# Performance work log

Measured on AMD Instinct MI355X. Metric: run time of the kernel, lower is better.

Reference implementation:

```python
import jax, jax.numpy as jnp
import numpy as np

B, S, D = 4, 2048, 256
H = 8
HD = D // H
DFF = 512
EPS_CUTOFF = 1e-15
LN_EPS = 1e-5


def _layer_norm(x, gamma, beta):
    mu = jnp.mean(x, axis=-1, keepdims=True)
    var = jnp.mean(jnp.square(x - mu), axis=-1, keepdims=True)
    return (x - mu) * jax.lax.rsqrt(var + LN_EPS) * gamma + beta


def setup_inputs() -> dict:
    key = jax.random.key(0)
    ks = jax.random.split(key, 12)
    s = 1.0 / np.sqrt(D)
    inp = {
        "tokens": jax.random.normal(ks[0], (B, S, D), dtype=jnp.float32),
        "cutoff_factors": jax.random.uniform(ks[1], (B, S, S), dtype=jnp.float32),
        "Wqkv": jax.random.uniform(ks[2], (3 * D, D), jnp.float32, -s, s),
        "bqkv": jnp.zeros((3 * D,), jnp.float32),
        "Wo": jax.random.uniform(ks[3], (D, D), jnp.float32, -s, s),
        "bo": jnp.zeros((D,), jnp.float32),
        "ln1_g": jnp.ones((D,), jnp.float32),
        "ln1_b": jnp.zeros((D,), jnp.float32),
        "ln2_g": jnp.ones((D,), jnp.float32),
        "ln2_b": jnp.zeros((D,), jnp.float32),
        "W1": jax.random.uniform(ks[4], (DFF, D), jnp.float32, -s, s),
        "b1": jax.random.uniform(ks[5], (DFF,), jnp.float32, -s, s),
        "W2": jax.random.uniform(ks[6], (D, DFF), jnp.float32, -1.0 / np.sqrt(DFF), 1.0 / np.sqrt(DFF)),
        "b2": jax.random.uniform(ks[7], (D,), jnp.float32, -1.0 / np.sqrt(DFF), 1.0 / np.sqrt(DFF)),
        "use_manual_attention": 1,
    }
    return inp


def reference(tokens, cutoff_factors, Wqkv, bqkv, Wo, bo, ln1_g, ln1_b, ln2_g, ln2_b, W1, b1, W2, b2, use_manual_attention):
    # --- attention block ---
    qkv = tokens @ Wqkv.T + bqkv                      # [B,S,3D]
    qkv = qkv.reshape(B, S, 3, H, HD).transpose(2, 0, 3, 1, 4)  # [3,B,H,S,HD]
    q, k, v = qkv[0], qkv[1], qkv[2]
    attn_mask = jnp.log(jnp.clip(cutoff_factors, EPS_CUTOFF))[:, None, :, :]  # [B,1,S,S]
    scores = jnp.einsum("bhqd,bhkd->bhqk", q, k) / np.sqrt(HD) + attn_mask
    probs = jax.nn.softmax(scores, axis=-1)
    attn = jnp.einsum("bhqk,bhkd->bhqd", probs, v)    # [B,H,S,HD]
    attn = attn.transpose(0, 2, 1, 3).reshape(B, S, D)
    attn = attn @ Wo.T + bo
    # --- PostLN residual + norm ---
    x = _layer_norm(tokens + attn, ln1_g, ln1_b)
    # --- MLP (SiLU) ---
    h = jax.nn.silu(x @ W1.T + b1)
    mlp_out = h @ W2.T + b2
    return _layer_norm(x + mlp_out, ln2_g, ln2_b)
```

## Files before the change

### kernel.cpp

```cpp
#include <hip/hip_runtime.h>
#include <hip/hip_bf16.h>
#include <math.h>

#define B_ 4
#define S_ 2048
#define D_ 256
#define H_ 8
#define HD_ 32
#define DFF_ 512

typedef __attribute__((ext_vector_type(8))) short bf16x8;
typedef __attribute__((ext_vector_type(4))) float f32x4;

__device__ inline short f2bf(float f) {
  union { float f; unsigned u; } x; x.f = f;
  unsigned r = (x.u + 0x7FFFu + ((x.u >> 16) & 1u)) >> 16;
  return (short)r;
}

__global__ __launch_bounds__(256) void cvt_f2bf(const float* __restrict__ src,
                                                short* __restrict__ dst, int n) {
  int i = (blockIdx.x * 256 + threadIdx.x) * 4;
  if (i < n) {
    float4 v = *(const float4*)(src + i);
    short4 s; s.x = f2bf(v.x); s.y = f2bf(v.y); s.z = f2bf(v.z); s.w = f2bf(v.w);
    *(short4*)(dst + i) = s;
  }
}

template<int MODE>
__global__ __launch_bounds__(256) void gemm_bf(const short* __restrict__ A,
                                               const short* __restrict__ W,
                                               const float* __restrict__ bias,
                                               float* __restrict__ Cf,
                                               short* __restrict__ Cb,
                                               int M, int N, int K) {
  constexpr int BM = 128, BN = 64;
  __shared__ short As[BM][72];
  __shared__ short Bs[BN][72];
  const int tid = threadIdx.x;
  const int wid = tid >> 6, lane = tid & 63;
  const int g = lane >> 4, lc = lane & 15;
  const int wr = wid >> 1, wc = wid & 1;
  const int rowBase = blockIdx.y * BM;
  const int colBase = blockIdx.x * BN;

  f32x4 acc[4][2];
#pragma unroll
  for (int m = 0; m < 4; ++m)
#pragma unroll
    for (int n = 0; n < 2; ++n) { acc[m][n][0]=0.f; acc[m][n][1]=0.f; acc[m][n][2]=0.f; acc[m][n][3]=0.f; }

  for (int k0 = 0; k0 < K; k0 += 64) {
    __syncthreads();
#pragma unroll
    for (int i = 0; i < 4; ++i) {
      int task = tid + 256 * i;
      int r = task >> 3, c = (task & 7) * 8;
      *(bf16x8*)&As[r][c] = *(const bf16x8*)(A + (size_t)(rowBase + r) * K + k0 + c);
    }
#pragma unroll
    for (int i = 0; i < 2; ++i) {
      int task = tid + 256 * i;
      int r = task >> 3, c = (task & 7) * 8;
      *(bf16x8*)&Bs[r][c] = *(const bf16x8*)(W + (size_t)(colBase + r) * K + k0 + c);
    }
    __syncthreads();
#pragma unroll
    for (int ks = 0; ks < 2; ++ks) {
      bf16x8 af[4], bfr[2];
#pragma unroll
      for (int m = 0; m < 4; ++m) af[m] = *(const bf16x8*)&As[wr*64 + m*16 + lc][ks*32 + g*8];
#pragma unroll
      for (int n = 0; n < 2; ++n) bfr[n] = *(const bf16x8*)&Bs[wc*32 + n*16 + lc][ks*32 + g*8];
#pragma unroll
      for (int m = 0; m < 4; ++m)
#pragma unroll
        for (int n = 0; n < 2; ++n)
          acc[m][n] = __builtin_amdgcn_mfma_f32_16x16x32_bf16(af[m], bfr[n], acc[m][n], 0, 0, 0);
    }
  }

#pragma unroll
  for (int m = 0; m < 4; ++m)
#pragma unroll
    for (int n = 0; n < 2; ++n) {
      int col = colBase + wc*32 + n*16 + lc;
      float bv = bias[col];
#pragma unroll
      for (int j = 0; j < 4; ++j) {
        int row = rowBase + wr*64 + m*16 + g*4 + j;
        float v = acc[m][n][j] + bv;
        if (MODE == 0) {
          Cf[(size_t)row * N + col] = v;
        } else if (MODE == 1) {
          v = v / (1.f + __expf(-v));
          Cb[(size_t)row * N + col] = f2bf(v);
        } else {
          int part = col >> 8;
          int h = (col >> 5) & 7;
          int hd = col & 31;
          int b = row >> 11, s = row & 2047;
          if (part == 0) v *= 0.17677669529663687f;
          Cb[(size_t)part * 2097152 + ((((size_t)b * 8 + h) * 2048 + s) * 32 + hd)] = f2bf(v);
        }
      }
    }
}

__global__ __launch_bounds__(512) void attn_mfma(const short* __restrict__ qkvbf,
                                                 const float* __restrict__ cutoff,
                                                 short* __restrict__ outbf) {
  constexpr int QB = 128, KB = 64;
  const int nqt = S_ / QB;
  const int qt = blockIdx.x % nqt;
  const int h  = (blockIdx.x / nqt) % H_;
  const int b  = blockIdx.x / (nqt * H_);
  const int tid = threadIdx.x;
  const int wid = tid >> 6;
  const int lane = tid & 63;
  const int g = lane >> 4, lc = lane & 15;

  __shared__ __align__(16) short Ks[KB][56];
  __shared__ __align__(16) short Vt[HD_][66];
  __shared__ __align__(16) short Plds[8][16][72];

  const int qbase = qt * QB + wid * 16;
  const size_t bh = ((size_t)b * H_ + h) * S_;
  const short* qg = qkvbf + bh * HD_;
  const short* kg = qkvbf + 2097152 + bh * HD_;
  const short* vg = qkvbf + 2 * 2097152 + bh * HD_;

  bf16x8 qf = *(const bf16x8*)(qg + (size_t)(qbase + lc) * HD_ + g * 8);

  f32x4 oacc[2];
#pragma unroll
  for (int d = 0; d < 2; ++d) { oacc[d][0]=0.f; oacc[d][1]=0.f; oacc[d][2]=0.f; oacc[d][3]=0.f; }
  float mx[4], sm[4];
#pragma unroll
  for (int r = 0; r < 4; ++r) { mx[r] = -1e30f; sm[r] = 0.f; }

  const float* cb = cutoff + ((size_t)(b * S_) + qbase + g * 4) * (size_t)S_ + lc;

  for (int kt = 0; kt < S_; kt += KB) {
    __syncthreads();
    if (tid < 256) {
      int r = tid >> 2, c = (tid & 3) * 8;
      *(bf16x8*)&Ks[r][c] = *(const bf16x8*)(kg + (size_t)(kt + r) * HD_ + c);
    } else {
      int tv = tid - 256;
      int r = tv >> 2, c = (tv & 3) * 8;
      bf16x8 vv = *(const bf16x8*)(vg + (size_t)(kt + r) * HD_ + c);
#pragma unroll
      for (int j = 0; j < 8; ++j) Vt[c + j][r] = vv[j];
    }
    __syncthreads();

    float cv[4][4];
#pragma unroll
    for (int n = 0; n < 4; ++n)
#pragma unroll
      for (int r = 0; r < 4; ++r)
        cv[n][r] = cb[(size_t)r * S_ + kt + n * 16];

    bf16x8 kf[4];
#pragma unroll
    for (int n = 0; n < 4; ++n) kf[n] = *(const bf16x8*)&Ks[n*16 + lc][g*8];
    f32x4 sc[4];
#pragma unroll
    for (int n = 0; n < 4; ++n) {
      f32x4 z = {0.f, 0.f, 0.f, 0.f};
      sc[n] = __builtin_amdgcn_mfma_f32_16x16x32_bf16(qf, kf[n], z, 0, 0, 0);
    }

    float nm[4], corr[4];
#pragma unroll
    for (int r = 0; r < 4; ++r) {
      float cm = fmaxf(fmaxf(sc[0][r], sc[1][r]), fmaxf(sc[2][r], sc[3][r]));
      cm = fmaxf(cm, __shfl_xor(cm, 1, 64));
      cm = fmaxf(cm, __shfl_xor(cm, 2, 64));
      cm = fmaxf(cm, __shfl_xor(cm, 4, 64));
      cm = fmaxf(cm, __shfl_xor(cm, 8, 64));
      nm[r] = fmaxf(mx[r], cm);
      corr[r] = __expf(mx[r] - nm[r]);
      mx[r] = nm[r];
    }
#pragma unroll
    for (int d = 0; d < 2; ++d)
#pragma unroll
      for (int r = 0; r < 4; ++r) oacc[d][r] *= corr[r];
    float rs[4] = {0.f, 0.f, 0.f, 0.f};
#pragma unroll
    for (int n = 0; n < 4; ++n)
#pragma unroll
      for (int r = 0; r < 4; ++r) {
        float p = fmaxf(cv[n][r], 1e-15f) * __expf(sc[n][r] - nm[r]);
        rs[r] += p;
        Plds[wid][g*4 + r][n*16 + lc] = f2bf(p);
      }
#pragma unroll
    for (int r = 0; r < 4; ++r) {
      float t = rs[r];
      t += __shfl_xor(t, 1, 64);
      t += __shfl_xor(t, 2, 64);
      t += __shfl_xor(t, 4, 64);
      t += __shfl_xor(t, 8, 64);
      sm[r] = sm[r] * corr[r] + t;
    }

    asm volatile("s_waitcnt lgkmcnt(0)" ::: "memory");
    __builtin_amdgcn_sched_barrier(0);

#pragma unroll
    for (int kh = 0; kh < 2; ++kh) {
      bf16x8 pa = *(const bf16x8*)&Plds[wid][lc][kh*32 + g*8];
#pragma unroll
      for (int d = 0; d < 2; ++d) {
        bf16x8 vb = *(const bf16x8*)&Vt[d*16 + lc][kh*32 + g*8];
        oacc[d] = __builtin_amdgcn_mfma_f32_16x16x32_bf16(pa, vb, oacc[d], 0, 0, 0);
      }
    }
  }

#pragma unroll
  for (int r = 0; r < 4; ++r) {
    float inv = 1.f / sm[r];
    int q = qbase + g*4 + r;
    short* op = outbf + ((size_t)(b * S_) + q) * D_ + h * HD_ + lc;
    op[0]  = f2bf(oacc[0][r] * inv);
    op[16] = f2bf(oacc[1][r] * inv);
  }
}

template<int WBF>
__global__ __launch_bounds__(256) void residual_ln(const float* __restrict__ xa,
                                                   const float* __restrict__ xb,
                                                   const float* __restrict__ g,
                                                   const float* __restrict__ bt,
                                                   float* __restrict__ out,
                                                   short* __restrict__ outbf) {
  const int row  = blockIdx.x * 4 + (threadIdx.x >> 6);
  const int lane = threadIdx.x & 63;
  float4 va = *(const float4*)(xa + (size_t)row * D_ + lane * 4);
  float4 vb = *(const float4*)(xb + (size_t)row * D_ + lane * 4);
  float v[4] = {va.x + vb.x, va.y + vb.y, va.z + vb.z, va.w + vb.w};
  float s = v[0] + v[1] + v[2] + v[3];
#pragma unroll
  for (int o = 32; o > 0; o >>= 1) s += __shfl_xor(s, o, 64);
  float mu = s * (1.f / D_);
  float var = 0.f;
#pragma unroll
  for (int i = 0; i < 4; ++i) { v[i] -= mu; var += v[i] * v[i]; }
#pragma unroll
  for (int o = 32; o > 0; o >>= 1) var += __shfl_xor(var, o, 64);
  float rs = rsqrtf(var * (1.f / D_) + 1e-5f);
  float4 g4 = *(const float4*)(g + lane * 4);
  float4 b4 = *(const float4*)(bt + lane * 4);
  float4 o4 = {v[0] * rs * g4.x + b4.x, v[1] * rs * g4.y + b4.y,
               v[2] * rs * g4.z + b4.z, v[3] * rs * g4.w + b4.w};
  *(float4*)(out + (size_t)row * D_ + lane * 4) = o4;
  if (WBF) {
    short4 s4; s4.x = f2bf(o4.x); s4.y = f2bf(o4.y); s4.z = f2bf(o4.z); s4.w = f2bf(o4.w);
    *(short4*)(outbf + (size_t)row * D_ + lane * 4) = s4;
  }
}

extern "C" void kernel_launch(void* const* d_in, const int* in_sizes, int n_in,
                              void* d_out, int out_size, void* d_ws, size_t ws_size,
                              hipStream_t stream) {
  const float* tokens = (const float*)d_in[0];
  const float* cutoff = (const float*)d_in[1];
  const float* Wqkv   = (const float*)d_in[2];
  const float* bqkv   = (const float*)d_in[3];
  const float* Wo     = (const float*)d_in[4];
  const float* bo     = (const float*)d_in[5];
  const float* ln1g   = (const float*)d_in[6];
  const float* ln1b   = (const float*)d_in[7];
  const float* ln2g   = (const float*)d_in[8];
  const float* ln2b   = (const float*)d_in[9];
  const float* W1     = (const float*)d_in[10];
  const float* b1     = (const float*)d_in[11];
  const float* W2     = (const float*)d_in[12];
  const float* b2     = (const float*)d_in[13];
  float* out = (float*)d_out;

  char* w = (char*)d_ws;
  const size_t MB = 1 << 20;
  short* qkvbf  = (short*)w;
  short* tokbf  = (short*)(w + 12 * MB);
  short* wq_bf  = (short*)(w + 16 * MB);
  short* wo_bf  = wq_bf + 196608;
  short* w1_bf  = wo_bf + 65536;
  short* w2_bf  = w1_bf + 131072;
  short* attnbf = tokbf;
  float* projOut = (float*)(w + 18 * MB);
  float* xbuf    = (float*)(w + 26 * MB);
  short* xbbf    = qkvbf;
  short* hbbf    = qkvbf + 2097152;
  float* mlpOut  = projOut;

  const int M = B_ * S_;

  cvt_f2bf<<<dim3(2048), 256, 0, stream>>>(tokens, tokbf, M * D_);
  cvt_f2bf<<<dim3(192),  256, 0, stream>>>(Wqkv, wq_bf, 3 * D_ * D_);
  cvt_f2bf<<<dim3(64),   256, 0, stream>>>(Wo,   wo_bf, D_ * D_);
  cvt_f2bf<<<dim3(128),  256, 0, stream>>>(W1,   w1_bf, DFF_ * D_);
  cvt_f2bf<<<dim3(128),  256, 0, stream>>>(W2,   w2_bf, D_ * DFF_);

  gemm_bf<2><<<dim3(12, 64), 256, 0, stream>>>(tokbf, wq_bf, bqkv, nullptr, qkvbf, M, 3 * D_, D_);
  attn_mfma<<<dim3(512), 512, 0, stream>>>(qkvbf, cutoff, attnbf);
  gemm_bf<0><<<dim3(4, 64), 256, 0, stream>>>(attnbf, wo_bf, bo, projOut, nullptr, M, D_, D_);
  residual_ln<1><<<dim3(M / 4), 256, 0, stream>>>(tokens, projOut, ln1g, ln1b, xbuf, xbbf);
  gemm_bf<1><<<dim3(8, 64), 256, 0, stream>>>(xbbf, w1_bf, b1, nullptr, hbbf, M, DFF_, D_);
  gemm_bf<0><<<dim3(4, 64), 256, 0, stream>>>(hbbf, w2_bf, b2, mlpOut, nullptr, M, D_, DFF_);
  residual_ln<0><<<dim3(M / 4), 256, 0, stream>>>(xbuf, mlpOut, ln2g, ln2b, out, nullptr);
}
```

Before: 172.4 us.

## Replace online softmax max with precomputed Cauchy-Schwarz bound per query

Adds a pre-pass kernel that computes, for each query, an upper bound on its scores (|q|·max|k|), and uses it as a fixed softmax offset in the attention kernel. This drops the per-tile running max, cross-lane max and sum shuffles, and accumulator rescaling. It also transposes the MFMA operands so each lane owns one query row, which gives vectorized float4 cutoff loads and packed bf16 stores. The risk is underflow: if true scores sit far below the bound, exp(s - m) can flush to zero. The extra pre-pass kernel adds a launch and a read of Q and K.

```diff
diff --git a/kernel.cpp b/kernel.cpp
--- a/kernel.cpp
+++ b/kernel.cpp
@@ -16,6 +16,15 @@
   union { float f; unsigned u; } x; x.f = f;
   unsigned r = (x.u + 0x7FFFu + ((x.u >> 16) & 1u)) >> 16;
   return (short)r;
+}
+__device__ inline float bf2f(short s) {
+  union { unsigned u; float f; } x; x.u = ((unsigned)(unsigned short)s) << 16;
+  return x.f;
+}
+__device__ inline unsigned cvt_pk_bf16(float a, float b) {
+  unsigned r;
+  asm("v_cvt_pk_bf16_f32 %0, %1, %2" : "=v"(r) : "v"(a), "v"(b));
+  return r;
 }
 
 __global__ __launch_bounds__(256) void cvt_f2bf(const float* __restrict__ src,
@@ -108,11 +117,51 @@
     }
 }
 
+__global__ __launch_bounds__(256) void calc_mfix(const short* __restrict__ qkvbf,
+                                                 float* __restrict__ mfix) {
+  const int bh = blockIdx.x;
+  const int t = threadIdx.x;
+  const short* qg = qkvbf + (size_t)bh * S_ * HD_;
+  const short* kg = qkvbf + 2097152 + (size_t)bh * S_ * HD_;
+  __shared__ float red[256];
+  float km2 = 0.f;
+  for (int r = t; r < S_; r += 256) {
+    const bf16x8* p = (const bf16x8*)(kg + (size_t)r * HD_);
+    float ss = 0.f;
+#pragma unroll
+    for (int c = 0; c < 4; ++c) {
+      bf16x8 v = p[c];
+#pragma unroll
+      for (int j = 0; j < 8; ++j) { float f = bf2f(v[j]); ss = fmaf(f, f, ss); }
+    }
+    km2 = fmaxf(km2, ss);
+  }
+  red[t] = km2;
+  __syncthreads();
+  for (int o = 128; o > 0; o >>= 1) {
+    if (t < o) red[t] = fmaxf(red[t], red[t + o]);
+    __syncthreads();
+  }
+  km2 = red[0];
+  for (int r = t; r < S_; r += 256) {
+    const bf16x8* p = (const bf16x8*)(qg + (size_t)r * HD_);
+    float ss = 0.f;
+#pragma unroll
+    for (int c = 0; c < 4; ++c) {
+      bf16x8 v = p[c];
+#pragma unroll
+      for (int j = 0; j < 8; ++j) { float f = bf2f(v[j]); ss = fmaf(f, f, ss); }
+    }
+    mfix[(size_t)bh * S_ + r] = sqrtf(ss * km2);
+  }
+}
+
 __global__ __launch_bounds__(512) void attn_mfma(const short* __restrict__ qkvbf,
                                                  const float* __restrict__ cutoff,
+                                                 const float* __restrict__ mfix,
                                                  short* __restrict__ outbf) {
-  constexpr int QB = 128, KB = 64;
-  const int nqt = S_ / QB;
+  constexpr int KB = 64;
+  const int nqt = S_ / 128;
   const int qt = blockIdx.x % nqt;
   const int h  = (blockIdx.x / nqt) % H_;
   const int b  = blockIdx.x / (nqt * H_);
@@ -123,24 +172,23 @@
 
   __shared__ __align__(16) short Ks[KB][56];
   __shared__ __align__(16) short Vt[HD_][66];
-  __shared__ __align__(16) short Plds[8][16][72];
-
-  const int qbase = qt * QB + wid * 16;
+  __shared__ __align__(16) short Pq[8][16][72];
+
+  const int qrow = qt * 128 + wid * 16 + lc;
   const size_t bh = ((size_t)b * H_ + h) * S_;
   const short* qg = qkvbf + bh * HD_;
   const short* kg = qkvbf + 2097152 + bh * HD_;
   const short* vg = qkvbf + 2 * 2097152 + bh * HD_;
 
-  bf16x8 qf = *(const bf16x8*)(qg + (size_t)(qbase + lc) * HD_ + g * 8);
+  bf16x8 qf = *(const bf16x8*)(qg + (size_t)qrow * HD_ + g * 8);
+  const float m = mfix[bh + qrow];
 
   f32x4 oacc[2];
 #pragma unroll
   for (int d = 0; d < 2; ++d) { oacc[d][0]=0.f; oacc[d][1]=0.f; oacc[d][2]=0.f; oacc[d][3]=0.f; }
-  float mx[4], sm[4];
-#pragma unroll
-  for (int r = 0; r < 4; ++r) { mx[r] = -1e30f; sm[r] = 0.f; }
-
-  const float* cb = cutoff + ((size_t)(b * S_) + qbase + g * 4) * (size_t)S_ + lc;
+  float sml = 0.f;
+
+  const float* cb = cutoff + ((size_t)(b * S_) + qrow) * (size_t)S_;
 
   for (int kt = 0; kt < S_; kt += KB) {
     __syncthreads();
@@ -156,56 +204,31 @@
     }
     __syncthreads();
 
-    float cv[4][4];
-#pragma unroll
-    for (int n = 0; n < 4; ++n)
-#pragma unroll
-      for (int r = 0; r < 4; ++r)
-        cv[n][r] = cb[(size_t)r * S_ + kt + n * 16];
+    float4 cv[4];
+#pragma unroll
+    for (int t = 0; t < 4; ++t) cv[t] = *(const float4*)(cb + kt + t * 16 + g * 4);
 
     bf16x8 kf[4];
 #pragma unroll
-    for (int n = 0; n < 4; ++n) kf[n] = *(const bf16x8*)&Ks[n*16 + lc][g*8];
-    f32x4 sc[4];
-#pragma unroll
-    for (int n = 0; n < 4; ++n) {
+    for (int t = 0; t < 4; ++t) kf[t] = *(const bf16x8*)&Ks[t*16 + lc][g*8];
+    f32x4 st[4];
+#pragma unroll
+    for (int t = 0; t < 4; ++t) {
       f32x4 z = {0.f, 0.f, 0.f, 0.f};
-      sc[n] = __builtin_amdgcn_mfma_f32_16x16x32_bf16(qf, kf[n], z, 0, 0, 0);
-    }
-
-    float nm[4], corr[4];
-#pragma unroll
-    for (int r = 0; r < 4; ++r) {
-      float cm = fmaxf(fmaxf(sc[0][r], sc[1][r]), fmaxf(sc[2][r], sc[3][r]));
-      cm = fmaxf(cm, __shfl_xor(cm, 1, 64));
-      cm = fmaxf(cm, __shfl_xor(cm, 2, 64));
-      cm = fmaxf(cm, __shfl_xor(cm, 4, 64));
-      cm = fmaxf(cm, __shfl_xor(cm, 8, 64));
-      nm[r] = fmaxf(mx[r], cm);
-      corr[r] = __expf(mx[r] - nm[r]);
-      mx[r] = nm[r];
-    }
-#pragma unroll
-    for (int d = 0; d < 2; ++d)
-#pragma unroll
-      for (int r = 0; r < 4; ++r) oacc[d][r] *= corr[r];
-    float rs[4] = {0.f, 0.f, 0.f, 0.f};
-#pragma unroll
-    for (int n = 0; n < 4; ++n)
-#pragma unroll
-      for (int r = 0; r < 4; ++r) {
-        float p = fmaxf(cv[n][r], 1e-15f) * __expf(sc[n][r] - nm[r]);
-        rs[r] += p;
-        Plds[wid][g*4 + r][n*16 + lc] = f2bf(p);
-      }
-#pragma unroll
-    for (int r = 0; r < 4; ++r) {
-      float t = rs[r];
-      t += __shfl_xor(t, 1, 64);
-      t += __shfl_xor(t, 2, 64);
-      t += __shfl_xor(t, 4, 64);
-      t += __shfl_xor(t, 8, 64);
-      sm[r] = sm[r] * corr[r] + t;
+      st[t] = __builtin_amdgcn_mfma_f32_16x16x32_bf16(kf[t], qf, z, 0, 0, 0);
+    }
+
+#pragma unroll
+    for (int t = 0; t < 4; ++t) {
+      float p0 = fmaxf(cv[t].x, 1e-15f) * __expf(st[t][0] - m);
+      float p1 = fmaxf(cv[t].y, 1e-15f) * __expf(st[t][1] - m);
+      float p2 = fmaxf(cv[t].z, 1e-15f) * __expf(st[t][2] - m);
+      float p3 = fmaxf(cv[t].w, 1e-15f) * __expf(st[t][3] - m);
+      sml += (p0 + p1) + (p2 + p3);
+      uint2 pk;
+      pk.x = cvt_pk_bf16(p0, p1);
+      pk.y = cvt_pk_bf16(p2, p3);
+      *(uint2*)&Pq[wid][lc][t*16 + g*4] = pk;
     }
 
     asm volatile("s_waitcnt lgkmcnt(0)" ::: "memory");
@@ -213,22 +236,26 @@
 
 #pragma unroll
     for (int kh = 0; kh < 2; ++kh) {
-      bf16x8 pa = *(const bf16x8*)&Plds[wid][lc][kh*32 + g*8];
-#pragma unroll
-      for (int d = 0; d < 2; ++d) {
-        bf16x8 vb = *(const bf16x8*)&Vt[d*16 + lc][kh*32 + g*8];
-        oacc[d] = __builtin_amdgcn_mfma_f32_16x16x32_bf16(pa, vb, oacc[d], 0, 0, 0);
+      bf16x8 pb = *(const bf16x8*)&Pq[wid][lc][kh*32 + g*8];
+#pragma unroll
+      for (int dh = 0; dh < 2; ++dh) {
+        bf16x8 va = *(const bf16x8*)&Vt[dh*16 + lc][kh*32 + g*8];
+        oacc[dh] = __builtin_amdgcn_mfma_f32_16x16x32_bf16(va, pb, oacc[dh], 0, 0, 0);
       }
     }
   }
 
-#pragma unroll
-  for (int r = 0; r < 4; ++r) {
-    float inv = 1.f / sm[r];
-    int q = qbase + g*4 + r;
-    short* op = outbf + ((size_t)(b * S_) + q) * D_ + h * HD_ + lc;
-    op[0]  = f2bf(oacc[0][r] * inv);
-    op[16] = f2bf(oacc[1][r] * inv);
+  float s = sml;
+  s += __shfl_xor(s, 16, 64);
+  s += __shfl_xor(s, 32, 64);
+  float inv = 1.f / s;
+
+#pragma unroll
+  for (int dh = 0; dh < 2; ++dh) {
+    uint2 pk;
+    pk.x = cvt_pk_bf16(oacc[dh][0] * inv, oacc[dh][1] * inv);
+    pk.y = cvt_pk_bf16(oacc[dh][2] * inv, oacc[dh][3] * inv);
+    *(uint2*)(outbf + ((size_t)(b * S_) + qrow) * D_ + h * HD_ + dh * 16 + g * 4) = pk;
   }
 }
 
@@ -295,6 +322,7 @@
   short* attnbf = tokbf;
   float* projOut = (float*)(w + 18 * MB);
   float* xbuf    = (float*)(w + 26 * MB);
+  float* mfix    = (float*)(w + 34 * MB);
   short* xbbf    = qkvbf;
   short* hbbf    = qkvbf + 2097152;
   float* mlpOut  = projOut;
@@ -308,7 +336,8 @@
   cvt_f2bf<<<dim3(128),  256, 0, stream>>>(W2,   w2_bf, D_ * DFF_);
 
   gemm_bf<2><<<dim3(12, 64), 256, 0, stream>>>(tokbf, wq_bf, bqkv, nullptr, qkvbf, M, 3 * D_, D_);
-  attn_mfma<<<dim3(512), 512, 0, stream>>>(qkvbf, cutoff, attnbf);
+  calc_mfix<<<dim3(32), 256, 0, stream>>>(qkvbf, mfix);
+  attn_mfma<<<dim3(512), 512, 0, stream>>>(qkvbf, cutoff, mfix, attnbf);
   gemm_bf<0><<<dim3(4, 64), 256, 0, stream>>>(attnbf, wo_bf, bo, projOut, nullptr, M, D_, D_);
   residual_ln<1><<<dim3(M / 4), 256, 0, stream>>>(tokens, projOut, ln1g, ln1b, xbuf, xbbf);
   gemm_bf<1><<<dim3(8, 64), 256, 0, stream>>>(xbbf, w1_bf, b1, nullptr, hbbf, M, DFF_, D_);
```

Result: faster. 153.9 us (-10.7%).
